# Kernel optimization log

Hardware: AMD Instinct MI355X
Metric: run time of the kernel (lower is better)

The kernel has to match this reference:

```python
import jax, jax.numpy as jnp
import numpy as np

EPS = 1e-12  # F.normalize default eps


def _unfold(x, k, pad, stride):
    # torch F.unfold: [B,C,H,W] -> [B, C*k*k, L], features ordered (c, kh, kw), L row-major.
    B, C, H, W = x.shape
    xp = jnp.pad(x, ((0, 0), (0, 0), (pad, pad), (pad, pad)))
    Ho = (H + 2 * pad - k) // stride + 1
    Wo = (W + 2 * pad - k) // stride + 1
    r = (jnp.arange(Ho) * stride)[:, None] + jnp.arange(k)[None, :]  # [Ho,k]
    c = (jnp.arange(Wo) * stride)[:, None] + jnp.arange(k)[None, :]  # [Wo,k]
    p = xp[:, :, r[:, None, :, None], c[None, :, None, :]]  # [B,C,Ho,Wo,k,k]
    return p.transpose(0, 1, 4, 5, 2, 3).reshape(B, C * k * k, Ho * Wo)


def _fold(p, out_hw, k, pad, stride):
    # torch F.fold: overlap-add inverse of _unfold.
    B, CKK, L = p.shape
    C = CKK // (k * k)
    H, W = out_hw
    Ho = (H + 2 * pad - k) // stride + 1
    Wo = (W + 2 * pad - k) // stride + 1
    p = p.reshape(B, C, k, k, Ho, Wo).transpose(0, 1, 4, 5, 2, 3)  # [B,C,Ho,Wo,k,k]
    r = (jnp.arange(Ho) * stride)[:, None] + jnp.arange(k)[None, :]
    c = (jnp.arange(Wo) * stride)[:, None] + jnp.arange(k)[None, :]
    out = jnp.zeros((B, C, H + 2 * pad, W + 2 * pad), p.dtype)
    out = out.at[:, :, r[:, None, :, None], c[None, :, None, :]].add(p)
    return out[:, :, pad:pad + H, pad:pad + W]


def _l2n(x, axis):
    n = jnp.sqrt(jnp.sum(x * x, axis=axis, keepdims=True))
    return x / jnp.maximum(n, EPS)


def setup_inputs() -> dict:
    key = jax.random.key(0)
    ks = jax.random.split(key, 11)
    B, H, W = 1, 32, 32
    f = jnp.float32
    return {
        'lrsr_lv3': jax.random.normal(ks[0], (B, 256, H, W), f),
        'refsr_lv1': jax.random.normal(ks[1], (B, 64, 4 * H, 4 * W), f),
        'refsr_lv2': jax.random.normal(ks[2], (B, 128, 2 * H, 2 * W), f),
        'refsr_lv3': jax.random.normal(ks[3], (B, 256, H, W), f),
        'ref_lv1': jax.random.normal(ks[4], (B, 64, 4 * H, 4 * W), f),
        'ref_lv2': jax.random.normal(ks[5], (B, 128, 2 * H, 2 * W), f),
        'ref_lv3': jax.random.normal(ks[6], (B, 256, H, W), f),
        'W1': jax.random.normal(ks[7], (2304, 1152), f) * 0.02,
        'b1': jax.random.normal(ks[8], (2304,), f) * 0.02,
        'W2': jax.random.normal(ks[9], (2304, 576), f) * 0.02,
        'b2': jax.random.normal(ks[10], (2304,), f) * 0.02,
    }


def reference(lrsr_lv3, refsr_lv1, refsr_lv2, refsr_lv3, ref_lv1, ref_lv2, ref_lv3, W1, b1, W2, b2):
    B, _, H, W = lrsr_lv3.shape
    lr3 = _unfold(lrsr_lv3, 3, 1, 1)                       # [B, 2304, N]
    r3 = _unfold(refsr_lv3, 3, 1, 1).transpose(0, 2, 1)    # [B, N3, 2304]
    r2 = _unfold(refsr_lv2, 3, 1, 1).transpose(0, 2, 1) @ W1.T + b1  # [B, N2, 2304]
    r1 = _unfold(refsr_lv1, 3, 1, 1).transpose(0, 2, 1) @ W2.T + b2  # [B, N1, 2304]
    r3 = _l2n(r3, 2); r2 = _l2n(r2, 2); r1 = _l2n(r1, 2)
    lr3 = _l2n(lr3, 1)
    R3 = jnp.einsum('bnd,bdm->bnm', r3, lr3)  # [B, N3, N]
    R2 = jnp.einsum('bnd,bdm->bnm', r2, lr3)  # [B, N2, N]
    R1 = jnp.einsum('bnd,bdm->bnm', r1, lr3)  # [B, N1, N]
    R3_star = jnp.max(R3, axis=1); R3_arg = jnp.argmax(R3, axis=1)
    R2_star = jnp.max(R2, axis=1)
    R1_star = jnp.max(R1, axis=1)
    ref3u = _unfold(ref_lv3, 3, 1, 1)
    ref2u = _unfold(ref_lv2, 6, 2, 2)
    ref1u = _unfold(ref_lv1, 12, 4, 4)
    idx = R3_arg[:, None, :]  # [B,1,N] broadcast over feature dim
    T3u = jnp.take_along_axis(ref3u, idx, axis=2)
    T2u = jnp.take_along_axis(ref2u, idx, axis=2)
    T1u = jnp.take_along_axis(ref1u, idx, axis=2)
    T_lv3 = _fold(T3u, (H, W), 3, 1, 1) / 9.0
    T_lv2 = _fold(T2u, (2 * H, 2 * W), 6, 2, 2) / 9.0
    T_lv1 = _fold(T1u, (4 * H, 4 * W), 12, 4, 4) / 9.0
    S_3 = R3_star.reshape(B, 1, H, W)
    S_2 = R2_star.reshape(B, 1, H, W)
    S_1 = R1_star.reshape(B, 1, H, W)
    return (S_1, S_2, S_3, T_lv3, T_lv2, T_lv1)
```

## Files before the change

### kernel.cpp

```cpp
#include <hip/hip_runtime.h>

typedef short bf8 __attribute__((ext_vector_type(8)));
typedef float f32x4 __attribute__((ext_vector_type(4)));

static __device__ __forceinline__ unsigned short f2bf(float f) {
  unsigned u = __float_as_uint(f);
  unsigned r = u + 0x7FFFu + ((u >> 16) & 1u);
  return (unsigned short)(r >> 16);
}
static __device__ __forceinline__ float bf2f(unsigned short h) {
  return __uint_as_float(((unsigned)h) << 16);
}
static __device__ __forceinline__ unsigned fkey(float f) {
  unsigned u = __float_as_uint(f);
  return (u & 0x80000000u) ? ~u : (u | 0x80000000u);
}
static __device__ __forceinline__ float kdec(unsigned k) {
  unsigned u = (k & 0x80000000u) ? (k & 0x7FFFFFFFu) : ~k;
  return __uint_as_float(u);
}
static __device__ __forceinline__ int xcdswz(int h, int nwg) {
  int q = nwg >> 3, r = nwg & 7;
  int xcd = h & 7, w = h >> 3;
  return (xcd < r ? xcd * (q + 1) : r * (q + 1) + (xcd - r) * q) + w;
}
static __device__ __forceinline__ int xcdbal(int h, int nwg, int nb0) {
  int xcd = h & 7, w = h >> 3;
  int qa = nb0 >> 3, qb = (nwg - nb0) >> 3;
  return (w < qa) ? (xcd * qa + w) : (nb0 + xcd * qb + (w - qa));
}
static __device__ __forceinline__ float win9s(const float* __restrict__ b, int m) {
  int mi = m >> 5, mj = m & 31;
  float s = 0.f;
#pragma unroll
  for (int dy = -1; dy <= 1; ++dy) {
    int i = mi + dy; if ((unsigned)i >= 32u) continue;
#pragma unroll
    for (int dx = -1; dx <= 1; ++dx) {
      int jx = mj + dx; if ((unsigned)jx >= 32u) continue;
      s += b[i * 32 + jx];
    }
  }
  return s;
}

static __device__ __forceinline__ void gload_lds16(const unsigned short* g, unsigned short* l) {
  __builtin_amdgcn_global_load_lds((const __attribute__((address_space(1))) void*)g,
                                   (__attribute__((address_space(3))) void*)l, 16, 0, 0);
}

static __device__ __forceinline__ float uf3(const float* __restrict__ src, int lgS, int d, int m) {
  const int S = 1 << lgS;
  int cc = d / 9;
  int r9 = d - cc * 9;
  int ki = r9 / 3;
  int kj = r9 - ki * 3;
  int i = (m >> lgS) + ki - 1;
  int j = (m & (S - 1)) + kj - 1;
  if ((unsigned)i >= (unsigned)S || (unsigned)j >= (unsigned)S) return 0.f;
  return src[((size_t)cc << (2 * lgS)) + ((size_t)i << lgS) + j];
}

__global__ __launch_bounds__(256) void k_prepA(const float* __restrict__ lrsr3, const float* __restrict__ rsr3,
                                               const float* __restrict__ rsr2, const float* __restrict__ rsr1,
                                               const float* __restrict__ W1, const float* __restrict__ W2,
                                               const float* __restrict__ b1, const float* __restrict__ b2,
                                               float* __restrict__ G2,
                                               float* __restrict__ rsr2t, float* __restrict__ rsr1t,
                                               unsigned short* __restrict__ lr3nbT,
                                               unsigned short* __restrict__ W1t, unsigned short* __restrict__ W2t,
                                               float* __restrict__ sclw, float* __restrict__ scu3w,
                                               float* __restrict__ D1, float* __restrict__ D2) {
  __shared__ __align__(16) unsigned char smem[18432];
  const int blk = blockIdx.x;
  const int tid = threadIdx.x;
  if (blk < 4) {
    float* b1L = (float*)smem;
    float* b2L = b1L + 2304;
    const int p = blk * 256 + tid;
    for (int i = tid; i < 2304; i += 256) { b1L[i] = b1[i]; b2L[i] = b2[i]; }
    __syncthreads();
    float d1a[9] = {}, d2a[9] = {};
    for (int cc = 0; cc < 256; ++cc) {
      float v = lrsr3[(size_t)cc * 1024 + p];
#pragma unroll
      for (int kk = 0; kk < 9; ++kk) {
        d1a[kk] = fmaf(b1L[cc * 9 + kk], v, d1a[kk]);
        d2a[kk] = fmaf(b2L[cc * 9 + kk], v, d2a[kk]);
      }
    }
#pragma unroll
    for (int kk = 0; kk < 9; ++kk) { D1[kk * 1024 + p] = d1a[kk]; D2[kk * 1024 + p] = d2a[kk]; }
  } else if (blk < 6) {
    float* ss = (float*)smem;
    const float* src = (blk == 4) ? lrsr3 : rsr3;
    float a4[4] = {0.f, 0.f, 0.f, 0.f};
    for (int cc = 0; cc < 256; ++cc) {
#pragma unroll
      for (int k = 0; k < 4; ++k) {
        float v = src[(size_t)cc * 1024 + k * 256 + tid];
        a4[k] = fmaf(v, v, a4[k]);
      }
    }
#pragma unroll
    for (int k = 0; k < 4; ++k) ss[k * 256 + tid] = a4[k];
    __syncthreads();
    float* dst = (blk == 4) ? sclw : scu3w;
#pragma unroll
    for (int k = 0; k < 4; ++k) {
      int m = k * 256 + tid;
      dst[m] = 1.f / fmaxf(sqrtf(win9s(ss, m)), 1e-12f);
    }
  } else if (blk < 1030) {
    float (*As)[32] = (float(*)[32])smem;
    float (*Bs)[32] = (float(*)[32])(smem + 2048);
    const int px = blk - 6;
    const int m0 = (px >> 5) * 32, n0 = (px & 31) * 32;
    const int tx = tid & 15, ty = tid >> 4;
    float acc[2][2] = {};
    for (int kb = 0; kb < 256; kb += 16) {
      __syncthreads();
      {
        int kk = tid >> 5, mm = tid & 31;
        As[kk][mm] = lrsr3[(size_t)(kb + kk) * 1024 + m0 + mm];
        Bs[kk][mm] = rsr3[(size_t)(kb + kk) * 1024 + n0 + mm];
        int e2 = tid + 256; int kk2 = e2 >> 5, mm2 = e2 & 31;
        As[kk2][mm2] = lrsr3[(size_t)(kb + kk2) * 1024 + m0 + mm2];
        Bs[kk2][mm2] = rsr3[(size_t)(kb + kk2) * 1024 + n0 + mm2];
      }
      __syncthreads();
#pragma unroll
      for (int kk = 0; kk < 16; ++kk) {
        float a0 = As[kk][ty * 2], a1 = As[kk][ty * 2 + 1];
        float b0 = Bs[kk][tx * 2], b1v = Bs[kk][tx * 2 + 1];
        acc[0][0] = fmaf(a0, b0, acc[0][0]); acc[0][1] = fmaf(a0, b1v, acc[0][1]);
        acc[1][0] = fmaf(a1, b0, acc[1][0]); acc[1][1] = fmaf(a1, b1v, acc[1][1]);
      }
    }
#pragma unroll
    for (int i = 0; i < 2; ++i)
#pragma unroll
      for (int jj = 0; jj < 2; ++jj)
        G2[(size_t)(m0 + ty * 2 + i) * 1024 + (n0 + tx * 2 + jj)] = acc[i][jj];
  } else if (blk < 1158) {
    float (*Tt)[65] = (float(*)[65])smem;
    const int idx = blk - 1030;
    const int ct = idx & 1, st = idx >> 1;
#pragma unroll
    for (int i = 0; i < 16; ++i) {
      int id = tid + i * 256;
      int r = id >> 6, c = id & 63;
      Tt[r][c] = rsr2[(size_t)(ct * 64 + r) * 4096 + st * 64 + c];
    }
    __syncthreads();
#pragma unroll
    for (int i = 0; i < 16; ++i) {
      int id = tid + i * 256;
      int cc2 = id >> 6, rr = id & 63;
      rsr2t[(size_t)(st * 64 + cc2) * 128 + ct * 64 + rr] = Tt[rr][cc2];
    }
  } else if (blk < 1414) {
    float (*Tt)[65] = (float(*)[65])smem;
    const int st = blk - 1158;
#pragma unroll
    for (int i = 0; i < 16; ++i) {
      int id = tid + i * 256;
      int r = id >> 6, c = id & 63;
      Tt[r][c] = rsr1[(size_t)r * 16384 + st * 64 + c];
    }
    __syncthreads();
#pragma unroll
    for (int i = 0; i < 16; ++i) {
      int id = tid + i * 256;
      int cc2 = id >> 6, rr = id & 63;
      rsr1t[(size_t)(st * 64 + cc2) * 64 + rr] = Tt[rr][cc2];
    }
  } else if (blk < 2566) {
    int id8 = (blk - 1414) * 256 + tid;
    int m = id8 / 288, c0 = (id8 - m * 288) * 8;
    bf8 v;
#pragma unroll
    for (int e = 0; e < 8; ++e) v[e] = (short)f2bf(uf3(lrsr3, 5, c0 + e, m));
    *(bf8*)(lr3nbT + (size_t)m * 2304 + c0) = v;
  } else {
    unsigned short (*Ls)[65] = (unsigned short(*)[65])smem;
    int idx = blk - 2566;
    int xx = idx % 27, yy = idx / 27;
    const float* W; unsigned short* Wt; int Cw, c0;
    if (xx < 18) { W = W1; Wt = W1t; Cw = 1152; c0 = xx * 64; }
    else         { W = W2; Wt = W2t; Cw = 576;  c0 = (xx - 18) * 64; }
    const int Cch = Cw / 9;
    const int d0 = yy * 64;
#pragma unroll
    for (int i = 0; i < 16; ++i) {
      int id = tid + i * 256;
      int r = id >> 6, c = id & 63;
      Ls[r][c] = f2bf(W[(size_t)(d0 + r) * Cw + c0 + c]);
    }
    __syncthreads();
#pragma unroll
    for (int i = 0; i < 16; ++i) {
      int id = tid + i * 256;
      int cc = id >> 6, rr = id & 63;
      int c = c0 + cc;
      Wt[(size_t)((c % 9) * Cch + c / 9) * 2304 + d0 + rr] = Ls[rr][cc];
    }
  }
}

struct Job {
  const unsigned short* Alo;
  const unsigned short* Ahi;
  const unsigned short* Bt;
  unsigned short* Clo;
  unsigned short* Chi;
  const float* bl;
  const float* bw;
  const float* bbp;
  const float* rowscale;
  float* pnsq;
  float* pbwd;
  float* cmax;
  int Msplit, N, K, nbx, Mtot, npart, which;
};

template <int EPI, int NBUF>
static __device__ __forceinline__ void gemm_body(const Job& j0, const Job& j1, int nb0, int bid,
                                                 unsigned char* smem) {
  unsigned short (*As)[128 * 64] = (unsigned short(*)[128 * 64])smem;
  unsigned short (*Bs)[128 * 64] = (unsigned short(*)[128 * 64])(smem + (size_t)NBUF * 16384);
  unsigned* colkey = (unsigned*)(smem + (size_t)2 * NBUF * 16384);
  float* ninvL = (float*)(smem + (size_t)2 * NBUF * 16384 + 512);

  const bool first = (bid < nb0);
  const Job j = first ? j0 : j1;
  const int local = bid - (first ? 0 : nb0);
  const int by = local / j.nbx;
  const int bx = local - by * j.nbx;
  const int m0 = by * 128, n0 = bx * 128;
  const int K = j.K, N = j.N;

  const unsigned short* Abase = (m0 < j.Msplit)
      ? j.Alo + (size_t)m0 * K
      : j.Ahi + (size_t)(m0 - j.Msplit) * K;

  const int tid = threadIdx.x;
  const int l = tid & 63;
  const int w = tid >> 6;
  const int wr = w >> 1, wc = w & 1;
  if (EPI == 2) {
    if (tid < 128) {
      colkey[tid] = 0u;
      const int r = m0 + tid;
      float nsq = 0.f, bwd = 0.f;
      for (int p = 0; p < j.npart; ++p) {
        nsq += j.pnsq[(size_t)p * j.Mtot + r];
        bwd += j.pbwd[(size_t)p * j.Mtot + r];
      }
      float tq = nsq + 2.f * bwd + j.bbp[j.which];
      ninvL[tid] = 1.f / fmaxf(sqrtf(fmaxf(tq, 0.f)), 1e-12f);
    }
  }

  f32x4 acc[4][4] = {};

  const int srow = w * 32;
  const int lrow = l >> 3;
  const int gcol = ((l & 7) ^ lrow) * 8;
  const int mr = l & 15;
  const int kg = l >> 4;

  const int nt = K >> 6;
  const int snap_kb = n0 + wc * 64;
  unsigned short snap[4][4][4];

  auto stage = [&](int buf, int kb) {
#pragma unroll
    for (int i = 0; i < 4; ++i) {
      int r = srow + i * 8;
      gload_lds16(Abase + (size_t)(r + lrow) * K + kb + gcol, &As[buf][r * 64]);
      gload_lds16(j.Bt + (size_t)(n0 + r + lrow) * K + kb + gcol, &Bs[buf][r * 64]);
    }
  };
  auto compute_tile = [&](int cur) {
#pragma unroll
    for (int ks = 0; ks < 2; ++ks) {
      bf8 af[4], bv[4];
#pragma unroll
      for (int mi = 0; mi < 4; ++mi) {
        const int row = wr * 64 + mi * 16 + mr;
        af[mi] = *(const bf8*)&As[cur][row * 64 + (((ks * 4 + kg) ^ (row & 7)) * 8)];
      }
#pragma unroll
      for (int ni = 0; ni < 4; ++ni) {
        const int row = wc * 64 + ni * 16 + mr;
        bv[ni] = *(const bf8*)&Bs[cur][row * 64 + (((ks * 4 + kg) ^ (row & 7)) * 8)];
      }
      __builtin_amdgcn_s_setprio(1);
#pragma unroll
      for (int mi = 0; mi < 4; ++mi)
#pragma unroll
        for (int ni = 0; ni < 4; ++ni)
          acc[mi][ni] = __builtin_amdgcn_mfma_f32_16x16x32_bf16(af[mi], bv[ni], acc[mi][ni], 0, 0, 0);
      __builtin_amdgcn_s_setprio(0);
    }
  };
  auto do_snap = [&](int cur) {
#pragma unroll
    for (int mi = 0; mi < 4; ++mi)
#pragma unroll
      for (int e = 0; e < 4; ++e) {
        const int row = wr * 64 + mi * 16 + kg * 4 + e;
#pragma unroll
        for (int ni = 0; ni < 4; ++ni) {
          const int slot = ni * 2 + (mr >> 3);
          snap[mi][ni][e] = As[cur][row * 64 + ((slot ^ (row & 7)) * 8) + (mr & 7)];
        }
      }
  };

  if constexpr (NBUF == 1) {
    for (int t = 0; t < nt; ++t) {
      if (t) __syncthreads();
      stage(0, t << 6);
      __syncthreads();
      compute_tile(0);
      if (EPI == 1 && (t << 6) == snap_kb) do_snap(0);
    }
  } else {
    auto waitv = [&](int Wt) {
      if (Wt >= 2)      asm volatile("s_waitcnt vmcnt(16)\ns_barrier" ::: "memory");
      else if (Wt == 1) asm volatile("s_waitcnt vmcnt(8)\ns_barrier" ::: "memory");
      else              asm volatile("s_waitcnt vmcnt(0)\ns_barrier" ::: "memory");
    };
#pragma unroll
    for (int p = 0; p < NBUF; ++p) if (p < nt) stage(p, p << 6);
    { int inflight = (NBUF < nt ? NBUF : nt); waitv(inflight - 1); }
    int cur = 0;
    for (int t = 0; t < nt; ++t) {
      compute_tile(cur);
      if (EPI == 1 && (t << 6) == snap_kb) do_snap(cur);
      if (t + 1 < nt) {
        asm volatile("s_waitcnt lgkmcnt(0)\ns_barrier" ::: "memory");
        if (t + NBUF < nt) stage(cur, (t + NBUF) << 6);
        const int im = (nt - 1 < t + NBUF) ? (nt - 1) : (t + NBUF);
        waitv(im - (t + 1));
        cur = (cur + 1 == NBUF) ? 0 : cur + 1;
      }
    }
  }

  const int lr0 = wr * 64;
  const int lc0 = wc * 64;
  if (EPI == 0) {
    const bool hi = (m0 >= j.Msplit);
    unsigned short* Cbase = hi ? j.Chi + (size_t)(m0 - j.Msplit) * N
                               : j.Clo + (size_t)m0 * N;
    float rs[4][4];
#pragma unroll
    for (int mi = 0; mi < 4; ++mi)
#pragma unroll
      for (int e = 0; e < 4; ++e)
        rs[mi][e] = hi ? j.rowscale[m0 - j.Msplit + lr0 + mi * 16 + kg * 4 + e] : 1.f;
#pragma unroll
    for (int mi = 0; mi < 4; ++mi)
#pragma unroll
      for (int ni = 0; ni < 4; ++ni)
#pragma unroll
        for (int e = 0; e < 4; ++e)
          Cbase[(size_t)(lr0 + mi * 16 + kg * 4 + e) * (size_t)N + (n0 + lc0 + ni * 16 + mr)] =
              f2bf(acc[mi][ni][e] * rs[mi][e]);
  } else if (EPI == 1) {
    float rp[4][4] = {};
    float bp[4][4] = {};
#pragma unroll
    for (int ni = 0; ni < 4; ++ni) {
      const float bwv = j.bw[n0 + lc0 + ni * 16 + mr];
#pragma unroll
      for (int mi = 0; mi < 4; ++mi)
#pragma unroll
        for (int e = 0; e < 4; ++e) {
          const float av = bf2f(snap[mi][ni][e]);
          rp[mi][e] += acc[mi][ni][e] * av;
          bp[mi][e] += bwv * av;
        }
    }
#pragma unroll
    for (int off = 1; off < 16; off <<= 1)
#pragma unroll
      for (int mi = 0; mi < 4; ++mi)
#pragma unroll
        for (int e = 0; e < 4; ++e) {
          rp[mi][e] += __shfl_xor(rp[mi][e], off);
          bp[mi][e] += __shfl_xor(bp[mi][e], off);
        }
    if (mr == 0) {
      const size_t slotbase = (size_t)(bx * 2 + wc) * j.Mtot;
#pragma unroll
      for (int mi = 0; mi < 4; ++mi)
#pragma unroll
        for (int e = 0; e < 4; ++e) {
          const int r = m0 + lr0 + mi * 16 + kg * 4 + e;
          j.pnsq[slotbase + r] = rp[mi][e];
          j.pbwd[slotbase + r] = bp[mi][e];
        }
    }
  } else {
    float nv[4][4];
#pragma unroll
    for (int mi = 0; mi < 4; ++mi)
#pragma unroll
      for (int e = 0; e < 4; ++e)
        nv[mi][e] = ninvL[lr0 + mi * 16 + kg * 4 + e];
#pragma unroll
    for (int ni = 0; ni < 4; ++ni) {
      float blv = j.bl[n0 + lc0 + ni * 16 + mr];
      float mx = -3.0e38f;
#pragma unroll
      for (int mi = 0; mi < 4; ++mi)
#pragma unroll
        for (int e = 0; e < 4; ++e) mx = fmaxf(mx, (acc[mi][ni][e] + blv) * nv[mi][e]);
      atomicMax(&colkey[lc0 + ni * 16 + mr], fkey(mx));
    }
    __syncthreads();
    if (tid < 128) j.cmax[(size_t)by * 1024 + n0 + tid] = kdec(colkey[tid]);
  }
}

__global__ __launch_bounds__(256) void k_prepBP(Job pa, Job pb, int nbP0,
                                                const float* __restrict__ rsr2t, const float* __restrict__ rsr1t,
                                                const float* __restrict__ W1, const float* __restrict__ W2,
                                                const float* __restrict__ b1, const float* __restrict__ b2,
                                                const float* __restrict__ sclw, const float* __restrict__ scu3w,
                                                const float* __restrict__ D1, const float* __restrict__ D2,
                                                const float* __restrict__ G2,
                                                unsigned short* __restrict__ U2b, unsigned short* __restrict__ U1b,
                                                float* __restrict__ bw2, float* __restrict__ bw1,
                                                float* __restrict__ bb,
                                                float* __restrict__ bl2, float* __restrict__ bl1,
                                                float* __restrict__ s3, int* __restrict__ arg) {
  __shared__ __align__(16) unsigned char sm[33792];
  const int blk = blockIdx.x;
  const int tid = threadIdx.x;
  if (blk < 218) {
    gemm_body<0, 1>(pa, pb, nbP0, xcdswz(blk, 218), sm);
  } else if (blk < 2522) {
    int id = (blk - 218) * 256 + tid;
    int t = id & 15, rest = id >> 4;
    int kk = rest % 9, n = rest / 9;
    int cc0 = t * 8;
    int ki = kk / 3, kj = kk - ki * 3;
    int sy = (n >> 6) + ki - 1, sx = (n & 63) + kj - 1;
    bf8 v;
    if ((unsigned)sy < 64u && (unsigned)sx < 64u) {
      const float* p = rsr2t + (size_t)(sy * 64 + sx) * 128 + cc0;
      f32x4 a = *(const f32x4*)p;
      f32x4 bq = *(const f32x4*)(p + 4);
#pragma unroll
      for (int e = 0; e < 4; ++e) { v[e] = (short)f2bf(a[e]); v[4 + e] = (short)f2bf(bq[e]); }
    } else {
#pragma unroll
      for (int e = 0; e < 8; ++e) v[e] = 0;
    }
    *(bf8*)(U2b + (size_t)n * 1152 + kk * 128 + cc0) = v;
  } else if (blk < 7642) {
    int id = (blk - 2522) * 256 + tid;
    int n = id / 80, rem = id - n * 80;
    int ks = rem >> 3, t = rem & 7;
    int cc0 = t * 8;
    bf8 v;
    if (ks == 9) {
#pragma unroll
      for (int e = 0; e < 8; ++e) v[e] = 0;
    } else {
      int ki = ks / 3, kj = ks - ki * 3;
      int sy = (n >> 7) + ki - 1, sx = (n & 127) + kj - 1;
      if ((unsigned)sy < 128u && (unsigned)sx < 128u) {
        const float* p = rsr1t + (size_t)(sy * 128 + sx) * 64 + cc0;
        f32x4 a = *(const f32x4*)p;
        f32x4 bq = *(const f32x4*)(p + 4);
#pragma unroll
        for (int e = 0; e < 4; ++e) { v[e] = (short)f2bf(a[e]); v[4 + e] = (short)f2bf(bq[e]); }
      } else {
#pragma unroll
        for (int e = 0; e < 8; ++e) v[e] = 0;
      }
    }
    *(bf8*)(U1b + (size_t)n * 640 + ks * 64 + cc0) = v;
  } else if (blk < 7722) {
    float* red = (float*)sm;
    int idx = blk - 7642;
    int x = idx & 7, y = idx >> 3;
    if (y == 9) {
      if (x >= 2) return;
      const float* b = x ? b2 : b1;
      float s = 0.f;
      for (int d = tid; d < 2304; d += 256) s += b[d] * b[d];
      red[tid] = s; __syncthreads();
      for (int o = 128; o > 0; o >>= 1) { if (tid < o) red[tid] += red[tid + o]; __syncthreads(); }
      if (tid == 0) bb[x] = red[0];
      return;
    }
    const bool two = x < 5;
    const float* W = two ? W1 : W2;
    const float* b = two ? b1 : b2;
    float* bw = two ? bw2 : bw1;
    const int Cw = two ? 1152 : 576;
    int c = (two ? x : x - 5) * 256 + tid;
    if (c >= Cw) return;
    int d0 = y * 256;
    float s = 0.f;
    for (int d = d0; d < d0 + 256; ++d) s += b[d] * W[(size_t)d * Cw + c];
    atomicAdd(&bw[(c % 9) * (Cw / 9) + c / 9], s);
  } else if (blk < 8746) {
    float* bv = (float*)sm;
    int* bidx = (int*)(sm + 1024);
    const int m = blk - 7722;
    const int mi = m >> 5, mj = m & 31;
    float best = -3.0e38f; int bi = 0;
    for (int n = tid; n < 1024; n += 256) {
      const int ni = n >> 5, nj = n & 31;
      float raw = 0.f;
#pragma unroll
      for (int dy = -1; dy <= 1; ++dy) {
#pragma unroll
        for (int dx = -1; dx <= 1; ++dx) {
          bool vm = ((unsigned)(mi + dy) < 32u) && ((unsigned)(mj + dx) < 32u);
          bool vn = ((unsigned)(ni + dy) < 32u) && ((unsigned)(nj + dx) < 32u);
          if (vm && vn) {
            int off = dy * 32 + dx;
            raw += G2[(size_t)(m + off) * 1024 + (n + off)];
          }
        }
      }
      float v = raw * scu3w[n];
      if (v > best) { best = v; bi = n; }
    }
    bv[tid] = best; bidx[tid] = bi;
    __syncthreads();
    for (int o = 128; o > 0; o >>= 1) {
      if (tid < o) {
        float ov = bv[tid + o]; int oi = bidx[tid + o];
        if (ov > bv[tid] || (ov == bv[tid] && oi < bidx[tid])) { bv[tid] = ov; bidx[tid] = oi; }
      }
      __syncthreads();
    }
    if (tid == 0) { s3[m] = bv[0] * sclw[m]; arg[m] = bidx[0]; }
  } else {
    int m = (blk - 8746) * 256 + tid;
    int mi = m >> 5, mj = m & 31;
    float a1 = 0.f, a2 = 0.f;
#pragma unroll
    for (int ki = 0; ki < 3; ++ki) {
      int i = mi + ki - 1; if ((unsigned)i >= 32u) continue;
#pragma unroll
      for (int kj = 0; kj < 3; ++kj) {
        int jx = mj + kj - 1; if ((unsigned)jx >= 32u) continue;
        int pix = i * 32 + jx;
        int kk = ki * 3 + kj;
        a1 += D1[kk * 1024 + pix];
        a2 += D2[kk * 1024 + pix];
      }
    }
    float sc = sclw[m];
    bl2[m] = a1 * sc;
    bl1[m] = a2 * sc;
  }
}

__global__ __launch_bounds__(256) void k_gE1(Job a, Job b, int nb0) {
  __shared__ __align__(16) unsigned char sm[33792];
  gemm_body<1, 1>(a, b, nb0, xcdbal((int)blockIdx.x, (int)gridDim.x, nb0), sm);
}
__global__ __launch_bounds__(256) void k_gE2(Job a, Job b, int nb0) {
  __shared__ __align__(16) unsigned char sm[33792];
  gemm_body<2, 1>(a, b, nb0, xcdbal((int)blockIdx.x, (int)gridDim.x, nb0), sm);
}

__global__ __launch_bounds__(256) void k_tfold(const float* __restrict__ ref3, const float* __restrict__ ref2,
                                               const float* __restrict__ ref1, const int* __restrict__ arg,
                                               const float* __restrict__ cmax1, const float* __restrict__ cmax2,
                                               float* __restrict__ out) {
  const int bid = blockIdx.x;
  const int tid = threadIdx.x;
  if (bid < 256) {
    __shared__ float plane[1024];
    __shared__ int argL[1024];
    const int c = bid;
#pragma unroll
    for (int k = 0; k < 4; ++k) {
      plane[k * 256 + tid] = ref3[(size_t)c * 1024 + k * 256 + tid];
      argL[k * 256 + tid] = arg[k * 256 + tid];
    }
    __syncthreads();
#pragma unroll
    for (int k = 0; k < 4; ++k) {
      int px = k * 256 + tid;
      int y = px >> 5, x = px & 31;
      float s = 0.f;
#pragma unroll
      for (int di = -1; di <= 1; ++di) {
        int i = y + di;
        if ((unsigned)i >= 32u) continue;
#pragma unroll
        for (int dj = -1; dj <= 1; ++dj) {
          int jw = x + dj;
          if ((unsigned)jw >= 32u) continue;
          int n2 = argL[i * 32 + jw];
          int rr = (n2 >> 5) + y - i, cc = (n2 & 31) + x - jw;
          if ((unsigned)rr < 32u && (unsigned)cc < 32u) s += plane[rr * 32 + cc];
        }
      }
      out[3072 + (size_t)c * 1024 + px] = s * (1.f / 9.f);
    }
  } else if (bid < 1280) {
    __shared__ int argL[1024];
#pragma unroll
    for (int k = 0; k < 4; ++k) argL[k * 256 + tid] = arg[k * 256 + tid];
    __syncthreads();
    int id2 = (bid - 256) * 256 + tid;
    int q = id2 & 31, y = (id2 >> 5) & 63, c = id2 >> 11;
    int iy = y >> 1;
    float s0 = 0.f, s1 = 0.f;
#pragma unroll
    for (int di = -1; di <= 1; ++di) {
      int i = iy + di;
      if ((unsigned)i >= 32u) continue;
      int ry = y - 2 * i;
#pragma unroll
      for (int dj = -1; dj <= 1; ++dj) {
        int jw = q + dj;
        if ((unsigned)jw >= 32u) continue;
        int n2 = argL[i * 32 + jw];
        int rr = (n2 >> 5) * 2 + ry;
        int cb = (n2 & 31) * 2 + 2 * (q - jw);
        if ((unsigned)rr < 64u && (unsigned)cb < 63u) {
          const float* p = ref2 + (size_t)c * 4096 + rr * 64 + cb;
          s0 += p[0]; s1 += p[1];
        }
      }
    }
    float2 o; o.x = s0 * (1.f / 9.f); o.y = s1 * (1.f / 9.f);
    *(float2*)(out + 265216 + (size_t)c * 4096 + y * 64 + 2 * q) = o;
  } else if (bid < 2304) {
    __shared__ int argL[1024];
#pragma unroll
    for (int k = 0; k < 4; ++k) argL[k * 256 + tid] = arg[k * 256 + tid];
    __syncthreads();
    int id1 = (bid - 1280) * 256 + tid;
    int q = id1 & 31, y = (id1 >> 5) & 127, c = id1 >> 12;
    int iy = y >> 2;
    f32x4 s = {0.f, 0.f, 0.f, 0.f};
#pragma unroll
    for (int di = -1; di <= 1; ++di) {
      int i = iy + di;
      if ((unsigned)i >= 32u) continue;
      int ry = y - 4 * i;
#pragma unroll
      for (int dj = -1; dj <= 1; ++dj) {
        int jw = q + dj;
        if ((unsigned)jw >= 32u) continue;
        int n2 = argL[i * 32 + jw];
        int rr = (n2 >> 5) * 4 + ry;
        int cb = (n2 & 31) * 4 + 4 * (q - jw);
        if ((unsigned)rr < 128u && (unsigned)cb < 125u) {
          f32x4 v = *(const f32x4*)(ref1 + (size_t)c * 16384 + rr * 128 + cb);
          s += v;
        }
      }
    }
    s *= (1.f / 9.f);
    *(f32x4*)(out + 789504 + (size_t)c * 16384 + y * 128 + 4 * q) = s;
  } else {
    int t = (bid - 2304) * 256 + tid;
    if (t < 1024) {
      float mx = -3.0e38f;
      for (int rb = 0; rb < 128; ++rb) mx = fmaxf(mx, cmax1[rb * 1024 + t]);
      out[t] = mx;
    } else {
      int tt = t - 1024;
      float mx = -3.0e38f;
      for (int rb = 0; rb < 32; ++rb) mx = fmaxf(mx, cmax2[rb * 1024 + tt]);
      out[1024 + tt] = mx;
    }
  }
}

static constexpr size_t OFF_BW2     = 0;
static constexpr size_t OFF_BW1     = 4608;
static constexpr size_t ZERO_BYTES  = 7168;
static constexpr size_t OFF_BB      = 7168;
static constexpr size_t OFF_BL2     = 7424;
static constexpr size_t OFF_BL1     = 11520;
static constexpr size_t OFF_SCLW    = 15616;
static constexpr size_t OFF_SCU3W   = 19712;
static constexpr size_t OFF_R3ARG   = 23808;
static constexpr size_t OFF_PNSQ2   = 27904;
static constexpr size_t OFF_PBWD2   = OFF_PNSQ2 + 294912;
static constexpr size_t OFF_PNSQ1   = OFF_PBWD2 + 294912;
static constexpr size_t OFF_PBWD1   = OFF_PNSQ1 + 655360;
static constexpr size_t OFF_CMAX2   = OFF_PBWD1 + 655360;
static constexpr size_t OFF_CMAX1   = OFF_CMAX2 + 131072;
static constexpr size_t OFF_LR3NBT  = OFF_CMAX1 + 524288;
static constexpr size_t OFF_U2B     = OFF_LR3NBT + 4718592;
static constexpr size_t OFF_U1B     = OFF_U2B    + 9437184;
static constexpr size_t OFF_W1T     = OFF_U1B    + 20971520;
static constexpr size_t OFF_W2T     = OFF_W1T    + 5308416;
static constexpr size_t OFF_A2      = OFF_W2T    + 2949120;
static constexpr size_t OFF_A1      = OFF_A2     + 2654208;
static constexpr size_t OFF_M2T     = OFF_A1     + 819200;
static constexpr size_t OFF_M1T     = OFF_M2T    + 2359296;
static constexpr size_t OFF_G2      = OFF_M1T    + 1310720;
static constexpr size_t OFF_R2T     = OFF_G2     + 4194304;
static constexpr size_t OFF_R1T     = OFF_R2T    + 2097152;
static constexpr size_t OFF_D1      = OFF_R1T    + 4194304;
static constexpr size_t OFF_D2      = OFF_D1     + 36864;

extern "C" void kernel_launch(void* const* d_in, const int* in_sizes, int n_in,
                              void* d_out, int out_size, void* d_ws, size_t ws_size,
                              hipStream_t stream) {
  (void)in_sizes; (void)n_in; (void)out_size; (void)ws_size;
  const float* lrsr3  = (const float*)d_in[0];
  const float* rsr1   = (const float*)d_in[1];
  const float* rsr2   = (const float*)d_in[2];
  const float* rsr3   = (const float*)d_in[3];
  const float* ref1   = (const float*)d_in[4];
  const float* ref2   = (const float*)d_in[5];
  const float* ref3   = (const float*)d_in[6];
  const float* W1     = (const float*)d_in[7];
  const float* b1     = (const float*)d_in[8];
  const float* W2     = (const float*)d_in[9];
  const float* b2     = (const float*)d_in[10];
  float* out = (float*)d_out;
  char* ws = (char*)d_ws;

  float*          bw2     = (float*)(ws + OFF_BW2);
  float*          bw1     = (float*)(ws + OFF_BW1);
  float*          bb      = (float*)(ws + OFF_BB);
  float*          bl2     = (float*)(ws + OFF_BL2);
  float*          bl1     = (float*)(ws + OFF_BL1);
  float*          sclw    = (float*)(ws + OFF_SCLW);
  float*          scu3w   = (float*)(ws + OFF_SCU3W);
  int*            R3arg   = (int*)(ws + OFF_R3ARG);
  float*          pnsq2   = (float*)(ws + OFF_PNSQ2);
  float*          pbwd2   = (float*)(ws + OFF_PBWD2);
  float*          pnsq1   = (float*)(ws + OFF_PNSQ1);
  float*          pbwd1   = (float*)(ws + OFF_PBWD1);
  float*          cmax2   = (float*)(ws + OFF_CMAX2);
  float*          cmax1   = (float*)(ws + OFF_CMAX1);
  unsigned short* lr3nbT  = (unsigned short*)(ws + OFF_LR3NBT);
  unsigned short* U2b     = (unsigned short*)(ws + OFF_U2B);
  unsigned short* U1b     = (unsigned short*)(ws + OFF_U1B);
  unsigned short* W1t     = (unsigned short*)(ws + OFF_W1T);
  unsigned short* W2t     = (unsigned short*)(ws + OFF_W2T);
  unsigned short* A2b     = (unsigned short*)(ws + OFF_A2);
  unsigned short* A1b     = (unsigned short*)(ws + OFF_A1);
  unsigned short* M2tb    = (unsigned short*)(ws + OFF_M2T);
  unsigned short* M1tb    = (unsigned short*)(ws + OFF_M1T);
  float*          G2      = (float*)(ws + OFF_G2);
  float*          rsr2t   = (float*)(ws + OFF_R2T);
  float*          rsr1t   = (float*)(ws + OFF_R1T);
  float*          D1      = (float*)(ws + OFF_D1);
  float*          D2      = (float*)(ws + OFF_D2);

  hipMemsetAsync(d_ws, 0, ZERO_BYTES, stream);
  hipMemsetAsync(ws + OFF_W2T + (size_t)576 * 2304 * 2, 0, (size_t)64 * 2304 * 2, stream);

  k_prepA<<<3538, 256, 0, stream>>>(lrsr3, rsr3, rsr2, rsr1, W1, W2, b1, b2,
                                    G2, rsr2t, rsr1t, lr3nbT, W1t, W2t, sclw, scu3w, D1, D2);

  Job jz = {};
  {
    Job a = jz, b = jz;
    a.Alo = W1t; a.Ahi = lr3nbT; a.Msplit = 1152; a.Bt = W1t;
    a.Clo = A2b; a.Chi = M2tb; a.rowscale = sclw; a.N = 1152; a.K = 2304; a.nbx = 9;
    b.Alo = W2t; b.Ahi = lr3nbT; b.Msplit = 640; b.Bt = W2t;
    b.Clo = A1b; b.Chi = M1tb; b.rowscale = sclw; b.N = 640; b.K = 2304; b.nbx = 5;
    k_prepBP<<<8750, 256, 0, stream>>>(a, b, 153, rsr2t, rsr1t, W1, W2, b1, b2,
                                       sclw, scu3w, D1, D2, G2,
                                       U2b, U1b, bw2, bw1, bb, bl2, bl1, out + 2048, R3arg);
  }
  {
    Job a = jz, b = jz;
    a.Alo = U2b; a.Ahi = U2b; a.Msplit = 4096; a.Bt = A2b;
    a.bw = bw2; a.pnsq = pnsq2; a.pbwd = pbwd2; a.Mtot = 4096;
    a.N = 1152; a.K = 1152; a.nbx = 9;
    b.Alo = U1b; b.Ahi = U1b; b.Msplit = 16384; b.Bt = A1b;
    b.bw = bw1; b.pnsq = pnsq1; b.pbwd = pbwd1; b.Mtot = 16384;
    b.N = 640; b.K = 640; b.nbx = 5;
    k_gE1<<<288 + 640, 256, 0, stream>>>(a, b, 288);
  }
  {
    Job a = jz, b = jz;
    a.Alo = U2b; a.Ahi = U2b; a.Msplit = 4096; a.Bt = M2tb;
    a.bl = bl2; a.pnsq = pnsq2; a.pbwd = pbwd2; a.bbp = bb;
    a.npart = 18; a.which = 0; a.cmax = cmax2; a.Mtot = 4096;
    a.N = 1024; a.K = 1152; a.nbx = 8;
    b.Alo = U1b; b.Ahi = U1b; b.Msplit = 16384; b.Bt = M1tb;
    b.bl = bl1; b.pnsq = pnsq1; b.pbwd = pbwd1; b.bbp = bb;
    b.npart = 10; b.which = 1; b.cmax = cmax1; b.Mtot = 16384;
    b.N = 1024; b.K = 640; b.nbx = 8;
    k_gE2<<<256 + 1024, 256, 0, stream>>>(a, b, 256);
  }

  k_tfold<<<2312, 256, 0, stream>>>(ref3, ref2, ref1, R3arg, cmax1, cmax2, out);
}
```

Baseline: 208.3 us.

## Permute bf16 feature layout to (kk,c) order and stage lrsr3 im2col in LDS

The lr3 im2col pack into bf16 now stages a row band of lrsr3 in shared memory and emits 8-wide vectors. It writes features in (kernel-offset, channel) order instead of per-element uf3 gathers from global memory. The W1/W2 transpose-pack is re-indexed so its feature dimension matches the new ordering, and the total prep block count drops. The goal is to cut redundant uncoalesced global reads in the prep kernel. Downstream GEMMs must agree on the permuted feature order, otherwise results would be wrong.

```diff
diff --git a/kernel.cpp b/kernel.cpp
--- a/kernel.cpp
+++ b/kernel.cpp
@@ -175,27 +175,54 @@
       int cc2 = id >> 6, rr = id & 63;
       rsr1t[(size_t)(st * 64 + cc2) * 64 + rr] = Tt[rr][cc2];
     }
-  } else if (blk < 2566) {
-    int id8 = (blk - 1414) * 256 + tid;
-    int m = id8 / 288, c0 = (id8 - m * 288) * 8;
-    bf8 v;
-#pragma unroll
-    for (int e = 0; e < 8; ++e) v[e] = (short)f2bf(uf3(lrsr3, 5, c0 + e, m));
-    *(bf8*)(lr3nbT + (size_t)m * 2304 + c0) = v;
+  } else if (blk < 1670) {
+    float (*Px)[33] = (float(*)[33])smem;
+    const int idx = blk - 1414;
+    const int y = idx >> 3;
+    const int cs = (idx & 7) * 32;
+    for (int e = tid; e < 3072; e += 256) {
+      int ccq = e / 96, p = e - ccq * 96;
+      int pix = (y - 1) * 32 + p;
+      Px[p][ccq] = ((unsigned)pix < 1024u) ? lrsr3[(size_t)(cs + ccq) * 1024 + pix] : 0.f;
+    }
+    __syncthreads();
+    for (int e8 = tid; e8 < 1152; e8 += 256) {
+      int ccq0 = (e8 & 3) * 8;
+      int r = e8 >> 2;
+      int kk = r % 9, mloc = r / 9;
+      int ki = kk / 3, kj = kk - ki * 3;
+      int xx2 = mloc + kj - 1;
+      bf8 v;
+      if ((unsigned)xx2 < 32u) {
+        const float* row = &Px[ki * 32 + xx2][ccq0];
+#pragma unroll
+        for (int e = 0; e < 8; ++e) v[e] = (short)f2bf(row[e]);
+      } else {
+#pragma unroll
+        for (int e = 0; e < 8; ++e) v[e] = 0;
+      }
+      *(bf8*)(lr3nbT + (size_t)(y * 32 + mloc) * 2304 + kk * 256 + cs + ccq0) = v;
+    }
   } else {
     unsigned short (*Ls)[65] = (unsigned short(*)[65])smem;
-    int idx = blk - 2566;
-    int xx = idx % 27, yy = idx / 27;
-    const float* W; unsigned short* Wt; int Cw, c0;
-    if (xx < 18) { W = W1; Wt = W1t; Cw = 1152; c0 = xx * 64; }
-    else         { W = W2; Wt = W2t; Cw = 576;  c0 = (xx - 18) * 64; }
+    int idx = blk - 1670;
+    const float* W; unsigned short* Wt; int Cw, c0, kk2, cb2;
+    if (idx < 648) {
+      W = W1; Wt = W1t; Cw = 1152;
+      int t3 = idx / 18; c0 = (idx % 18) * 64;
+      kk2 = t3 >> 2; cb2 = (t3 & 3) * 64;
+    } else {
+      idx -= 648;
+      W = W2; Wt = W2t; Cw = 576;
+      int t3 = idx / 9; c0 = (idx % 9) * 64;
+      kk2 = t3 >> 2; cb2 = (t3 & 3) * 64;
+    }
     const int Cch = Cw / 9;
-    const int d0 = yy * 64;
 #pragma unroll
     for (int i = 0; i < 16; ++i) {
       int id = tid + i * 256;
       int r = id >> 6, c = id & 63;
-      Ls[r][c] = f2bf(W[(size_t)(d0 + r) * Cw + c0 + c]);
+      Ls[r][c] = f2bf(W[(size_t)((cb2 + r) * 9 + kk2) * Cw + c0 + c]);
     }
     __syncthreads();
 #pragma unroll
@@ -203,7 +230,7 @@
       int id = tid + i * 256;
       int cc = id >> 6, rr = id & 63;
       int c = c0 + cc;
-      Wt[(size_t)((c % 9) * Cch + c / 9) * 2304 + d0 + rr] = Ls[rr][cc];
+      Wt[(size_t)((c % 9) * Cch + c / 9) * 2304 + kk2 * 256 + cb2 + rr] = Ls[rr][cc];
     }
   }
 }
@@ -766,7 +793,7 @@
   hipMemsetAsync(d_ws, 0, ZERO_BYTES, stream);
   hipMemsetAsync(ws + OFF_W2T + (size_t)576 * 2304 * 2, 0, (size_t)64 * 2304 * 2, stream);
 
-  k_prepA<<<3538, 256, 0, stream>>>(lrsr3, rsr3, rsr2, rsr1, W1, W2, b1, b2,
+  k_prepA<<<2642, 256, 0, stream>>>(lrsr3, rsr3, rsr2, rsr1, W1, W2, b1, b2,
                                     G2, rsr2t, rsr1t, lr3nbT, W1t, W2t, sclw, scu3w, D1, D2);
 
   Job jz = {};
```

Measured after the change: 205.5 us, median of 2. No clear change (-1.4%).
